# Kernel tuning notes

Measured on AMD Instinct MI355X. Metric: run time of the kernel, lower is better.

The kernel has to match this reference:

```python
import jax, jax.numpy as jnp
import numpy as np

# RVQECell configuration (matches init_kwargs)
I_SZ, W_SZ, STAGES, ORDER, DEGREE = 6, 12, 3, 2, 2
BIAS = float(np.pi / 2)
ANC = ORDER - 1                      # ancillas_for_order(order) = order - 1
N = I_SZ + W_SZ + ANC                # 19 qubits
B = 32
INOUT = list(range(I_SZ))            # lanes 0..5
WORK = list(range(I_SZ, I_SZ + W_SZ))  # lanes 6..17
C_CTRL = I_SZ + W_SZ - 1             # controls per neuron = 17


def setup_inputs() -> dict:
    key = jax.random.key(0)
    ks = jax.random.split(key, 9)
    s = 0.1  # small init keeps neuron angles in a well-conditioned range
    psi = jax.random.normal(ks[0], (B, 2 ** N), jnp.float32)
    psi = psi / jnp.linalg.norm(psi, axis=1, keepdims=True)  # normalized kets
    return {
        "batch": psi,
        "w_in1": jax.random.normal(ks[1], (W_SZ, C_CTRL), jnp.float32) * s,
        "w_in2": jax.random.normal(ks[2], (W_SZ, C_CTRL, C_CTRL), jnp.float32) * s,
        "w_u": jax.random.normal(ks[3], (STAGES, W_SZ), jnp.float32) * s,
        "w_k1": jax.random.normal(ks[4], (STAGES, W_SZ, C_CTRL), jnp.float32) * s,
        "w_k2": jax.random.normal(ks[5], (STAGES, W_SZ, C_CTRL, C_CTRL), jnp.float32) * s,
        "w_out1": jax.random.normal(ks[6], (I_SZ, C_CTRL), jnp.float32) * s,
        "w_out2": jax.random.normal(ks[7], (I_SZ, C_CTRL, C_CTRL), jnp.float32) * s,
        "inputs": jax.random.randint(ks[8], (B, I_SZ), 0, 2, dtype=jnp.int32),
    }


def _rot_y(state, lane, alpha):
    # real rotation [[cos a, -sin a], [sin a, cos a]] on qubit `lane`.
    ax = lane + 1  # +1 for batch axis; state shape [B] + [2]*N
    c, s = jnp.cos(alpha), jnp.sin(alpha)
    p0 = jax.lax.index_in_dim(state, 0, ax, keepdims=True)
    p1 = jax.lax.index_in_dim(state, 1, ax, keepdims=True)
    return jnp.concatenate([c * p0 - s * p1, s * p0 + c * p1], axis=ax)


def _neuron(state, outlane, th1, th2):
    # Fast (deterministic RUS) quantum neuron of given ORDER/DEGREE:
    # per control-basis-branch rotation of `outlane` by alpha(x),
    # phi(x) = bias + sum_i th1_i x_i + sum_{i<j} th2_ij x_i x_j (degree 2),
    # alpha = q^(order-1)(phi), q(t) = arctan(tan(t)^2), stable via arctan2.
    controls = [l for l in range(I_SZ + W_SZ) if l != outlane]
    Cn = len(controls)
    x = jnp.arange(2 ** Cn)
    shifts = jnp.arange(Cn - 1, -1, -1)
    bits = ((x[:, None] >> shifts[None, :]) & 1).astype(state.dtype)  # [2^Cn, Cn]
    phi = BIAS + bits @ th1
    if DEGREE >= 2:
        phi = phi + jnp.einsum('xi,ij,xj->x', bits, jnp.triu(th2, 1), bits)
    alpha = phi
    for _ in range(ORDER - 1):
        alpha = jnp.arctan2(jnp.sin(alpha) ** 2, jnp.cos(alpha) ** 2)
    shape = [1] + [2 if l in controls else 1 for l in range(N)]
    return _rot_y(state, outlane, alpha.reshape(shape))


def _bitflip(state_flat, inputs):
    # Vectorized batched BitFlipLayer: X on inout lane i where inputs[b,i]==1,
    # i.e. permute amplitudes by XOR of the flip mask (lane 0 most significant).
    shifts = (N - 1) - jnp.arange(I_SZ)
    f = jnp.sum(inputs.astype(jnp.int32) << shifts[None, :], axis=1)  # [B]
    idx = jnp.arange(2 ** N, dtype=jnp.int32)[None, :] ^ f[:, None]
    return jnp.take_along_axis(state_flat, idx, axis=1)


def reference(batch, w_in1, w_in2, w_u, w_k1, w_k2, w_out1, w_out2, inputs):
    psi = _bitflip(batch, inputs).reshape((B,) + (2,) * N)
    # input layer: one neuron per workspace lane
    for j, out in enumerate(WORK):
        psi = _neuron(psi, out, w_in1[j], w_in2[j])
    # kernel layer: stages x (UnitaryLayer(workspace) + neurons)
    for st in range(STAGES):
        for j, lane in enumerate(WORK):
            psi = _rot_y(psi, lane, w_u[st, j])
        for j, out in enumerate(WORK):
            psi = _neuron(psi, out, w_k1[st, j], w_k2[st, j])
    psi = _bitflip(psi.reshape(B, -1), inputs).reshape((B,) + (2,) * N)
    # output layer: one neuron per inout lane
    for j, out in enumerate(INOUT):
        psi = _neuron(psi, out, w_out1[j], w_out2[j])
    # measurement probabilities over inout lanes: marginal of |amp|^2
    probs = jnp.sum(psi ** 2, axis=tuple(range(1 + I_SZ, 1 + N))).reshape(B, -1)
    return probs, psi.reshape(B, -1)
```

## Files before the change

kernel.cpp:

```cpp
#include <hip/hip_runtime.h>
#include <math.h>


#define BIAS_F 1.57079632679489662f

typedef float v4f __attribute__((ext_vector_type(4)));

__device__ __forceinline__ float4 ntload4(const float* p) {
    v4f v = __builtin_nontemporal_load((const v4f*)p);
    return make_float4(v.x, v.y, v.z, v.w);
}
__device__ __forceinline__ void ntstore4(float* p, float4 f) {
    v4f v = {f.x, f.y, f.z, f.w};
    __builtin_nontemporal_store(v, (v4f*)p);
}

__device__ __forceinline__ int SW(int i) { return i ^ ((i >> 3) & 0x1C); }
__device__ __forceinline__ float4 ldsld4(const float* st, int i) {
    return *(const float4*)&st[SW(i)];
}
__device__ __forceinline__ void ldsst4(float* st, int i, float4 v) {
    *(float4*)&st[SW(i)] = v;
}

#define LD2(p) (*(const float2*)(p))
#define LD4(p) (*(const float4*)(p))

__device__ __forceinline__ void rot4(float4& A, float4& B, float4 e) {
    float ax = A.x, ay = A.y, az = A.z, aw = A.w;
    A.x = e.x * ax - e.y * B.x;  B.x = e.y * ax + e.x * B.x;
    A.y = e.x * ay - e.y * B.y;  B.y = e.y * ay + e.x * B.y;
    A.z = e.z * az - e.w * B.z;  B.z = e.w * az + e.z * B.z;
    A.w = e.z * aw - e.w * B.w;  B.w = e.w * aw + e.z * B.w;
}
__device__ __forceinline__ void rotq(float4& P, float c, float s) {
    float px = P.x, py = P.y;
    P.x = c * px - s * P.z;  P.z = s * px + c * P.z;
    P.y = c * py - s * P.w;  P.w = s * py + c * P.w;
}


__global__ __launch_bounds__(256) void tables_kernel(
    const float* __restrict__ w_in1, const float* __restrict__ w_in2,
    const float* __restrict__ w_k1,  const float* __restrict__ w_k2,
    const float* __restrict__ w_out1, const float* __restrict__ w_out2,
    float* __restrict__ tab)
{
    const int n = blockIdx.y;
    const int hi = blockIdx.x;
    const int tid = threadIdx.x;
    const float* th1;
    const float* th2;
    if (n < 12)      { th1 = w_in1 + n * 17;         th2 = w_in2 + n * 289; }
    else if (n < 48) { th1 = w_k1 + (n - 12) * 17;   th2 = w_k2 + (n - 12) * 289; }
    else             { th1 = w_out1 + (n - 48) * 17; th2 = w_out2 + (n - 48) * 289; }

    float phi_hi = BIAS_F;
    float C[8];
#pragma unroll
    for (int a = 0; a < 8; ++a) C[a] = th1[9 + a];
#pragma unroll
    for (int i = 0; i < 9; ++i) {
        if ((hi >> (8 - i)) & 1) {
            float acc = th1[i];
#pragma unroll
            for (int j = i + 1; j < 9; ++j)
                if ((hi >> (8 - j)) & 1) acc += th2[i * 17 + j];
            phi_hi += acc;
#pragma unroll
            for (int a = 0; a < 8; ++a) C[a] += th2[i * 17 + 9 + a];
        }
    }

    float bt[8];
#pragma unroll
    for (int j = 0; j < 8; ++j) bt[j] = (float)((tid >> (7 - j)) & 1);
    float phi = phi_hi;
#pragma unroll
    for (int a = 0; a < 8; ++a) {
        float acc = C[a];
#pragma unroll
        for (int b2 = a + 1; b2 < 8; ++b2) acc += bt[b2] * th2[(9 + a) * 17 + 9 + b2];
        phi += bt[a] * acc;
    }

    float sp, cp;
    sincosf(phi, &sp, &cp);
    float c2 = cp * cp, s2 = sp * sp;
    float d = c2 * c2 + s2 * s2;
    float r = rsqrtf(d);
    r = r * (1.5f - 0.5f * d * r * r);
    float2* dst = (float2*)tab + ((size_t)n * 131072 + (size_t)((hi << 8) | tid));
    *dst = make_float2(c2 * r, s2 * r);
}

template <int PA, bool NEUR>
__device__ __forceinline__ void pass_hi2(float* l0, float* l1, int t8,
    const float* tA, const float* tB, const float* tC,
    float cA, float sA, float cB, float sB, float cC, float sC)
{
    const int lowb = PA - 4;
    const int low = t8 & ((1 << lowb) - 1);
    const int high = t8 >> lowb;
    const int i0 = (high << (PA + 1)) | (low << 2);
    const int x0 = (high << (PA - 1)) | (low << 1);
    const int oa = 1 << PA, ob = oa >> 1, oc = oa >> 2;
    const int dhi = oa >> 2, dlo = oa >> 3;
    float4 ea00, ea01, ea10, ea11, eb00, eb01, eb10, eb11, ec00, ec01, ec10, ec11;
    if (NEUR) {
        ea00 = LD4(&tA[2 * x0]);            ea01 = LD4(&tA[2 * (x0 + dlo)]);
        ea10 = LD4(&tA[2 * (x0 + dhi)]);    ea11 = LD4(&tA[2 * (x0 + dhi + dlo)]);
        eb00 = LD4(&tB[2 * x0]);            eb01 = LD4(&tB[2 * (x0 + dlo)]);
        eb10 = LD4(&tB[2 * (x0 + dhi)]);    eb11 = LD4(&tB[2 * (x0 + dhi + dlo)]);
        ec00 = LD4(&tC[2 * x0]);            ec01 = LD4(&tC[2 * (x0 + dlo)]);
        ec10 = LD4(&tC[2 * (x0 + dhi)]);    ec11 = LD4(&tC[2 * (x0 + dhi + dlo)]);
    } else {
        ea00 = ea01 = ea10 = ea11 = make_float4(cA, sA, cA, sA);
        eb00 = eb01 = eb10 = eb11 = make_float4(cB, sB, cB, sB);
        ec00 = ec01 = ec10 = ec11 = make_float4(cC, sC, cC, sC);
    }
#pragma unroll
    for (int s = 0; s < 2; ++s) {
        float* sl = (s == 0) ? l0 : l1;
        float4 Q000 = ldsld4(sl, i0),            Q001 = ldsld4(sl, i0 + oc);
        float4 Q010 = ldsld4(sl, i0 + ob),       Q011 = ldsld4(sl, i0 + ob + oc);
        float4 Q100 = ldsld4(sl, i0 + oa),       Q101 = ldsld4(sl, i0 + oa + oc);
        float4 Q110 = ldsld4(sl, i0 + oa + ob),  Q111 = ldsld4(sl, i0 + oa + ob + oc);
        rot4(Q000, Q100, ea00); rot4(Q001, Q101, ea01);
        rot4(Q010, Q110, ea10); rot4(Q011, Q111, ea11);
        rot4(Q000, Q010, eb00); rot4(Q001, Q011, eb01);
        rot4(Q100, Q110, eb10); rot4(Q101, Q111, eb11);
        rot4(Q000, Q001, ec00); rot4(Q010, Q011, ec01);
        rot4(Q100, Q101, ec10); rot4(Q110, Q111, ec11);
        ldsst4(sl, i0, Q000);            ldsst4(sl, i0 + oc, Q001);
        ldsst4(sl, i0 + ob, Q010);       ldsst4(sl, i0 + ob + oc, Q011);
        ldsst4(sl, i0 + oa, Q100);       ldsst4(sl, i0 + oa + oc, Q101);
        ldsst4(sl, i0 + oa + ob, Q110);  ldsst4(sl, i0 + oa + ob + oc, Q111);
    }
}

template <bool NEUR>
__device__ __forceinline__ void pass_lo2(float* l0, float* l1, int t8,
    const float* tA, const float* tB, const float* tC,
    float cA, float sA, float cB, float sB, float cC, float sC)
{
    const int i0 = t8 << 5, x0 = t8 << 3;
    float4 ea0, ea1, ea2, ea3, eb0, eb1, eb2, eb3, ec0, ec1, ec2, ec3;
    if (NEUR) {
        ea0 = LD4(&tA[2 * x0]);      ea1 = LD4(&tA[2 * x0 + 4]);
        ea2 = LD4(&tA[2 * x0 + 8]);  ea3 = LD4(&tA[2 * x0 + 12]);
        eb0 = LD4(&tB[2 * x0]);      eb1 = LD4(&tB[2 * x0 + 4]);
        eb2 = LD4(&tB[2 * x0 + 8]);  eb3 = LD4(&tB[2 * x0 + 12]);
        ec0 = LD4(&tC[2 * x0]);      ec1 = LD4(&tC[2 * x0 + 4]);
        ec2 = LD4(&tC[2 * x0 + 8]);  ec3 = LD4(&tC[2 * x0 + 12]);
    } else {
        ea0 = ea1 = ea2 = ea3 = make_float4(cA, sA, cA, sA);
        eb0 = eb1 = eb2 = eb3 = make_float4(cB, sB, cB, sB);
        ec0 = ec1 = ec2 = ec3 = make_float4(cC, sC, cC, sC);
    }
#pragma unroll
    for (int s = 0; s < 2; ++s) {
        float* sl = (s == 0) ? l0 : l1;
        float4 Q0 = ldsld4(sl, i0),      Q1 = ldsld4(sl, i0 + 4);
        float4 Q2 = ldsld4(sl, i0 + 8),  Q3 = ldsld4(sl, i0 + 12);
        float4 Q4 = ldsld4(sl, i0 + 16), Q5 = ldsld4(sl, i0 + 20);
        float4 Q6 = ldsld4(sl, i0 + 24), Q7 = ldsld4(sl, i0 + 28);
        rot4(Q0, Q2, ea0); rot4(Q1, Q3, ea1); rot4(Q4, Q6, ea2); rot4(Q5, Q7, ea3);
        rot4(Q0, Q1, eb0); rot4(Q2, Q3, eb1); rot4(Q4, Q5, eb2); rot4(Q6, Q7, eb3);
        rotq(Q0, ec0.x, ec0.y); rotq(Q1, ec0.z, ec0.w);
        rotq(Q2, ec1.x, ec1.y); rotq(Q3, ec1.z, ec1.w);
        rotq(Q4, ec2.x, ec2.y); rotq(Q5, ec2.z, ec2.w);
        rotq(Q6, ec3.x, ec3.y); rotq(Q7, ec3.z, ec3.w);
        ldsst4(sl, i0, Q0);      ldsst4(sl, i0 + 4, Q1);
        ldsst4(sl, i0 + 8, Q2);  ldsst4(sl, i0 + 12, Q3);
        ldsst4(sl, i0 + 16, Q4); ldsst4(sl, i0 + 20, Q5);
        ldsst4(sl, i0 + 24, Q6); ldsst4(sl, i0 + 28, Q7);
    }
}

__global__ __launch_bounds__(256, 2) void main_kernel(
    const float* __restrict__ batch, const float* __restrict__ w_u,
    const int* __restrict__ inputs, const float* __restrict__ tab,
    float* __restrict__ psi, float* __restrict__ probs)
{
    __shared__ __align__(16) float lds[2][8192];
    const int t8 = threadIdx.x;
    const int blk = blockIdx.x;
    const int xcd = blk & 7;
    const int vt = (xcd << 3) | ((blk >> 3) & 7);
    const int pair = blk >> 6;

    if (blk == 0) {
        float4 z = make_float4(0.f, 0.f, 0.f, 0.f);
        *(float4*)&probs[t8 * 8] = z;
        *(float4*)&probs[t8 * 8 + 4] = z;
    }

    int bb[2], uu[2];
#pragma unroll
    for (int s = 0; s < 2; ++s) {
        int b = pair * 2 + s;
        int fb = 0;
#pragma unroll
        for (int i = 0; i < 6; ++i) fb |= (inputs[b * 6 + i] & 1) << (5 - i);
        bb[s] = b; uu[s] = vt ^ fb;
        const float* src = batch + ((size_t)b << 19) + ((size_t)uu[s] << 13);
#pragma unroll
        for (int k = 0; k < 8; ++k) {
            int i4 = (k * 256 + t8) * 4;
            float4 v = ntload4(&src[i4]);
            *(float4*)&lds[s][SW(i4)] = v;
        }
    }
    float* l0 = lds[0];
    float* l1 = lds[1];

    const float* tb = tab + ((size_t)vt << 12);
#define TN(j) (tb + (size_t)(j) * 262144)
#define BAR __syncthreads()
    BAR;
    pass_hi2<12, true>(l0, l1, t8, TN(0), TN(1), TN(2), 0,0,0,0,0,0);  BAR;
    pass_hi2<9,  true>(l0, l1, t8, TN(3), TN(4), TN(5), 0,0,0,0,0,0);  BAR;
    pass_hi2<6,  true>(l0, l1, t8, TN(6), TN(7), TN(8), 0,0,0,0,0,0);  BAR;
    pass_lo2<true>(l0, l1, t8, TN(9), TN(10), TN(11), 0,0,0,0,0,0);    BAR;

#pragma unroll 1
    for (int st2 = 0; st2 < 3; ++st2) {
        const float* wu = w_u + st2 * 12;
        float c0, s0, c1, s1, c2, s2;
        sincosf(wu[0], &s0, &c0); sincosf(wu[1], &s1, &c1); sincosf(wu[2], &s2, &c2);
        pass_hi2<12, false>(l0, l1, t8, 0,0,0, c0,s0, c1,s1, c2,s2);   BAR;
        sincosf(wu[3], &s0, &c0); sincosf(wu[4], &s1, &c1); sincosf(wu[5], &s2, &c2);
        pass_hi2<9, false>(l0, l1, t8, 0,0,0, c0,s0, c1,s1, c2,s2);    BAR;
        sincosf(wu[6], &s0, &c0); sincosf(wu[7], &s1, &c1); sincosf(wu[8], &s2, &c2);
        pass_hi2<6, false>(l0, l1, t8, 0,0,0, c0,s0, c1,s1, c2,s2);    BAR;
        sincosf(wu[9], &s0, &c0); sincosf(wu[10], &s1, &c1); sincosf(wu[11], &s2, &c2);
        pass_lo2<false>(l0, l1, t8, 0,0,0, c0,s0, c1,s1, c2,s2);       BAR;

        const int nb = 12 + st2 * 12;
        pass_hi2<12, true>(l0, l1, t8, TN(nb+0), TN(nb+1), TN(nb+2), 0,0,0,0,0,0); BAR;
        pass_hi2<9,  true>(l0, l1, t8, TN(nb+3), TN(nb+4), TN(nb+5), 0,0,0,0,0,0); BAR;
        pass_hi2<6,  true>(l0, l1, t8, TN(nb+6), TN(nb+7), TN(nb+8), 0,0,0,0,0,0); BAR;
        pass_lo2<true>(l0, l1, t8, TN(nb+9), TN(nb+10), TN(nb+11), 0,0,0,0,0,0);   BAR;
    }
#undef TN
#undef BAR

#pragma unroll
    for (int s = 0; s < 2; ++s) {
        float* dst = psi + ((size_t)bb[s] << 19) + ((size_t)uu[s] << 13);
#pragma unroll
        for (int k = 0; k < 8; ++k) {
            int i4 = (k * 256 + t8) * 4;
            float4 v = *(const float4*)&lds[s][SW(i4)];
            ntstore4(&dst[i4], v);
        }
    }
}

__global__ __launch_bounds__(256, 2) void out_kernel(
    const float* __restrict__ tab, float* __restrict__ psi,
    float* __restrict__ probs)
{
    __shared__ __align__(16) float ts[16384];
    const int tid = threadIdx.x;
    const int lane = tid & 63;
    const int wv = tid >> 6;
    const int b = blockIdx.x >> 5;
    const int c0 = (blockIdx.x & 31) << 8;
    float* gbase = psi + ((size_t)b << 19) + c0;

#pragma unroll
    for (int i = 0; i < 16; ++i) {
        int k = wv * 16 + i;
        float4 v = ntload4(&gbase[((size_t)k << 13) + lane * 4]);
        int f4 = lane ^ (k & 15);
        *(float4*)&ts[k * 256 + f4 * 4] = v;
    }
    __syncthreads();

    float a[64];
#pragma unroll
    for (int k = 0; k < 64; ++k) a[k] = ts[k * 256 + (tid ^ ((k & 15) << 2))];
    const int w12 = (c0 | tid) >> 1;

#define OSTAGE(J) { \
    const float* tj = tab + 2u * ((size_t)(48 + (J)) * 131072 + (size_t)w12); \
    _Pragma("unroll") \
    for (int h = 0; h < 2; ++h) { \
        float2 ev[16]; \
        _Pragma("unroll") \
        for (int m = 0; m < 16; ++m) ev[m] = LD2(&tj[(size_t)(h * 16 + m) << 13]); \
        _Pragma("unroll") \
        for (int m = 0; m < 16; ++m) { \
            const int mm = h * 16 + m; \
            const int q = 5 - (J); \
            const int k0 = ((mm >> q) << (q + 1)) | (mm & ((1 << q) - 1)); \
            const int k1 = k0 | (1 << q); \
            float2 e = ev[m]; \
            float A0 = a[k0], A1 = a[k1]; \
            a[k0] = e.x * A0 - e.y * A1; \
            a[k1] = e.y * A0 + e.x * A1; } } }
    OSTAGE(0) OSTAGE(1) OSTAGE(2) OSTAGE(3) OSTAGE(4) OSTAGE(5)
#undef OSTAGE

#pragma unroll
    for (int k = 0; k < 64; ++k) ts[k * 256 + (tid ^ ((k & 15) << 2))] = a[k];
    __syncthreads();

#pragma unroll
    for (int i = 0; i < 16; ++i) {
        int k = wv * 16 + i;
        int f4 = lane ^ (k & 15);
        float4 v = *(const float4*)&ts[k * 256 + f4 * 4];
        ntstore4(&gbase[((size_t)k << 13) + lane * 4], v);
    }

    const int k6 = tid & 63, seg = tid >> 6;
    float p = 0.f;
#pragma unroll
    for (int j = 0; j < 64; ++j) {
        int c = seg * 64 + ((j + k6) & 63);
        float v = ts[k6 * 256 + (c ^ ((k6 & 15) << 2))];
        p += v * v;
    }
    atomicAdd(&probs[b * 64 + k6], p);
}

extern "C" void kernel_launch(void* const* d_in, const int* in_sizes, int n_in,
                              void* d_out, int out_size, void* d_ws, size_t ws_size,
                              hipStream_t stream)
{
    const float* batch  = (const float*)d_in[0];
    const float* w_in1  = (const float*)d_in[1];
    const float* w_in2  = (const float*)d_in[2];
    const float* w_u    = (const float*)d_in[3];
    const float* w_k1   = (const float*)d_in[4];
    const float* w_k2   = (const float*)d_in[5];
    const float* w_out1 = (const float*)d_in[6];
    const float* w_out2 = (const float*)d_in[7];
    const int*   inputs = (const int*)d_in[8];
    float* probs = (float*)d_out;
    float* psi   = (float*)d_out + 2048;
    float* tab   = (float*)d_ws;

    tables_kernel<<<dim3(512, 54), 256, 0, stream>>>(w_in1, w_in2, w_k1, w_k2,
                                                     w_out1, w_out2, tab);
    main_kernel<<<1024, 256, 0, stream>>>(batch, w_u, inputs, tab, psi, probs);
    out_kernel<<<1024, 256, 0, stream>>>(tab, psi, probs);
}
```

Measured before the change: 328.3 us.

## Relayout output-neuron tables for coalesced LDS staging and batch table rows per block

The output-layer neuron tables are written in a transposed, rotated layout so that out_kernel can load two stages' tables with contiguous float4 copies into shared memory and read them from LDS. Before, each thread did strided global float2 loads. The tables kernel also now has each block loop over 8 high-index rows, which cuts its grid by 8x. This adds extra barriers in out_kernel and reuses the ts buffer, and the smaller table grid may lower occupancy.

```diff
diff --git a/kernel.cpp b/kernel.cpp
--- a/kernel.cpp
+++ b/kernel.cpp
@@ -47,7 +47,7 @@
     float* __restrict__ tab)
 {
     const int n = blockIdx.y;
-    const int hi = blockIdx.x;
+    const int bx = blockIdx.x;
     const int tid = threadIdx.x;
     const float* th1;
     const float* th2;
@@ -55,43 +55,57 @@
     else if (n < 48) { th1 = w_k1 + (n - 12) * 17;   th2 = w_k2 + (n - 12) * 289; }
     else             { th1 = w_out1 + (n - 48) * 17; th2 = w_out2 + (n - 48) * 289; }
 
-    float phi_hi = BIAS_F;
-    float C[8];
-#pragma unroll
-    for (int a = 0; a < 8; ++a) C[a] = th1[9 + a];
-#pragma unroll
-    for (int i = 0; i < 9; ++i) {
-        if ((hi >> (8 - i)) & 1) {
-            float acc = th1[i];
-#pragma unroll
-            for (int j = i + 1; j < 9; ++j)
-                if ((hi >> (8 - j)) & 1) acc += th2[i * 17 + j];
-            phi_hi += acc;
-#pragma unroll
-            for (int a = 0; a < 8; ++a) C[a] += th2[i * 17 + 9 + a];
-        }
-    }
-
     float bt[8];
 #pragma unroll
     for (int j = 0; j < 8; ++j) bt[j] = (float)((tid >> (7 - j)) & 1);
-    float phi = phi_hi;
-#pragma unroll
-    for (int a = 0; a < 8; ++a) {
-        float acc = C[a];
-#pragma unroll
-        for (int b2 = a + 1; b2 < 8; ++b2) acc += bt[b2] * th2[(9 + a) * 17 + 9 + b2];
-        phi += bt[a] * acc;
-    }
-
-    float sp, cp;
-    sincosf(phi, &sp, &cp);
-    float c2 = cp * cp, s2 = sp * sp;
-    float d = c2 * c2 + s2 * s2;
-    float r = rsqrtf(d);
-    r = r * (1.5f - 0.5f * d * r * r);
-    float2* dst = (float2*)tab + ((size_t)n * 131072 + (size_t)((hi << 8) | tid));
-    *dst = make_float2(c2 * r, s2 * r);
+
+#pragma unroll 1
+    for (int k = 0; k < 8; ++k) {
+        const int hi = bx * 8 + k;
+
+        float phi_hi = BIAS_F;
+        float C[8];
+#pragma unroll
+        for (int a = 0; a < 8; ++a) C[a] = th1[9 + a];
+#pragma unroll
+        for (int i = 0; i < 9; ++i) {
+            if ((hi >> (8 - i)) & 1) {
+                float acc = th1[i];
+#pragma unroll
+                for (int j = i + 1; j < 9; ++j)
+                    if ((hi >> (8 - j)) & 1) acc += th2[i * 17 + j];
+                phi_hi += acc;
+#pragma unroll
+                for (int a = 0; a < 8; ++a) C[a] += th2[i * 17 + 9 + a];
+            }
+        }
+
+        float phi = phi_hi;
+#pragma unroll
+        for (int a = 0; a < 8; ++a) {
+            float acc = C[a];
+#pragma unroll
+            for (int b2 = a + 1; b2 < 8; ++b2) acc += bt[b2] * th2[(9 + a) * 17 + 9 + b2];
+            phi += bt[a] * acc;
+        }
+
+        float sp, cp;
+        sincosf(phi, &sp, &cp);
+        float c2 = cp * cp, s2 = sp * sp;
+        float d = c2 * c2 + s2 * s2;
+        float r = rsqrtf(d);
+        r = r * (1.5f - 0.5f * d * r * r);
+
+        size_t idx;
+        if (n < 48) {
+            idx = (size_t)n * 131072 + (size_t)((hi << 8) | tid);
+        } else {
+            const int m = hi >> 4;
+            const int w12 = ((hi & 15) << 8) | tid;
+            idx = (size_t)n * 131072 + (size_t)(w12 * 32 + ((m + w12) & 31));
+        }
+        ((float2*)tab)[idx] = make_float2(c2 * r, s2 * r);
+    }
 }
 
 template <int PA, bool NEUR>
@@ -282,28 +296,44 @@
     float a[64];
 #pragma unroll
     for (int k = 0; k < 64; ++k) a[k] = ts[k * 256 + (tid ^ ((k & 15) << 2))];
-    const int w12 = (c0 | tid) >> 1;
-
-#define OSTAGE(J) { \
-    const float* tj = tab + 2u * ((size_t)(48 + (J)) * 131072 + (size_t)w12); \
+
+    const int w12l = tid >> 1;
+    const size_t tbase = (size_t)(c0 >> 1) * 32;
+    const float2* tab2 = (const float2*)tab;
+    float2* ts2 = (float2*)ts;
+
+#define OSTAGE(J, TSEL) { \
+    const int q = 5 - (J); \
     _Pragma("unroll") \
-    for (int h = 0; h < 2; ++h) { \
-        float2 ev[16]; \
-        _Pragma("unroll") \
-        for (int m = 0; m < 16; ++m) ev[m] = LD2(&tj[(size_t)(h * 16 + m) << 13]); \
-        _Pragma("unroll") \
-        for (int m = 0; m < 16; ++m) { \
-            const int mm = h * 16 + m; \
-            const int q = 5 - (J); \
-            const int k0 = ((mm >> q) << (q + 1)) | (mm & ((1 << q) - 1)); \
-            const int k1 = k0 | (1 << q); \
-            float2 e = ev[m]; \
-            float A0 = a[k0], A1 = a[k1]; \
-            a[k0] = e.x * A0 - e.y * A1; \
-            a[k1] = e.y * A0 + e.x * A1; } } }
-    OSTAGE(0) OSTAGE(1) OSTAGE(2) OSTAGE(3) OSTAGE(4) OSTAGE(5)
+    for (int m = 0; m < 32; ++m) { \
+        float2 e = ts2[(TSEL) * 4096 + w12l * 32 + ((m + w12l) & 31)]; \
+        const int k0 = ((m >> q) << (q + 1)) | (m & ((1 << q) - 1)); \
+        const int k1 = k0 | (1 << q); \
+        float A0 = a[k0], A1 = a[k1]; \
+        a[k0] = e.x * A0 - e.y * A1; \
+        a[k1] = e.y * A0 + e.x * A1; } }
+
+#pragma unroll 1
+    for (int p = 0; p < 3; ++p) {
+        __syncthreads();
+        const float4* g0 = (const float4*)(tab2 + (size_t)(48 + 2 * p) * 131072 + tbase);
+        const float4* g1 = (const float4*)(tab2 + (size_t)(49 + 2 * p) * 131072 + tbase);
+        float4* d4 = (float4*)ts;
+#pragma unroll 4
+        for (int it = 0; it < 8; ++it) {
+            d4[it * 256 + tid]        = g0[it * 256 + tid];
+            d4[2048 + it * 256 + tid] = g1[it * 256 + tid];
+        }
+        __syncthreads();
+        switch (p) {
+            case 0: OSTAGE(0, 0) OSTAGE(1, 1) break;
+            case 1: OSTAGE(2, 0) OSTAGE(3, 1) break;
+            default: OSTAGE(4, 0) OSTAGE(5, 1) break;
+        }
+    }
 #undef OSTAGE
 
+    __syncthreads();
 #pragma unroll
     for (int k = 0; k < 64; ++k) ts[k * 256 + (tid ^ ((k & 15) << 2))] = a[k];
     __syncthreads();
@@ -344,8 +374,8 @@
     float* psi   = (float*)d_out + 2048;
     float* tab   = (float*)d_ws;
 
-    tables_kernel<<<dim3(512, 54), 256, 0, stream>>>(w_in1, w_in2, w_k1, w_k2,
-                                                     w_out1, w_out2, tab);
+    tables_kernel<<<dim3(64, 54), 256, 0, stream>>>(w_in1, w_in2, w_k1, w_k2,
+                                                    w_out1, w_out2, tab);
     main_kernel<<<1024, 256, 0, stream>>>(batch, w_u, inputs, tab, psi, probs);
     out_kernel<<<1024, 256, 0, stream>>>(tab, psi, probs);
 }
```

Result: slower. 374.4 us (+14.1%).

## Fuse three kernels into persistent mega-kernel with software grid barriers

Applied to the files above, without the earlier changes.

Merges the table-building, main state-evolution and output-neuron kernels into a single persistent kernel of 512 blocks. Each block does two work units per phase, and atomic-counter grid barriers (reset by a memset) separate the phases. The aim is to remove kernel launch gaps and tail effects between the three launches. In exchange, occupancy is halved relative to 1024-block launches, and correctness depends on all 512 blocks being co-resident; if they are not, the barriers deadlock. Table computation now loops over 54 neurons serially per block.

```diff
diff --git a/kernel.cpp b/kernel.cpp
--- a/kernel.cpp
+++ b/kernel.cpp
@@ -39,60 +39,17 @@
     P.y = c * py - s * P.w;  P.w = s * py + c * P.w;
 }
 
-
-__global__ __launch_bounds__(256) void tables_kernel(
-    const float* __restrict__ w_in1, const float* __restrict__ w_in2,
-    const float* __restrict__ w_k1,  const float* __restrict__ w_k2,
-    const float* __restrict__ w_out1, const float* __restrict__ w_out2,
-    float* __restrict__ tab)
-{
-    const int n = blockIdx.y;
-    const int hi = blockIdx.x;
-    const int tid = threadIdx.x;
-    const float* th1;
-    const float* th2;
-    if (n < 12)      { th1 = w_in1 + n * 17;         th2 = w_in2 + n * 289; }
-    else if (n < 48) { th1 = w_k1 + (n - 12) * 17;   th2 = w_k2 + (n - 12) * 289; }
-    else             { th1 = w_out1 + (n - 48) * 17; th2 = w_out2 + (n - 48) * 289; }
-
-    float phi_hi = BIAS_F;
-    float C[8];
-#pragma unroll
-    for (int a = 0; a < 8; ++a) C[a] = th1[9 + a];
-#pragma unroll
-    for (int i = 0; i < 9; ++i) {
-        if ((hi >> (8 - i)) & 1) {
-            float acc = th1[i];
-#pragma unroll
-            for (int j = i + 1; j < 9; ++j)
-                if ((hi >> (8 - j)) & 1) acc += th2[i * 17 + j];
-            phi_hi += acc;
-#pragma unroll
-            for (int a = 0; a < 8; ++a) C[a] += th2[i * 17 + 9 + a];
-        }
-    }
-
-    float bt[8];
-#pragma unroll
-    for (int j = 0; j < 8; ++j) bt[j] = (float)((tid >> (7 - j)) & 1);
-    float phi = phi_hi;
-#pragma unroll
-    for (int a = 0; a < 8; ++a) {
-        float acc = C[a];
-#pragma unroll
-        for (int b2 = a + 1; b2 < 8; ++b2) acc += bt[b2] * th2[(9 + a) * 17 + 9 + b2];
-        phi += bt[a] * acc;
-    }
-
-    float sp, cp;
-    sincosf(phi, &sp, &cp);
-    float c2 = cp * cp, s2 = sp * sp;
-    float d = c2 * c2 + s2 * s2;
-    float r = rsqrtf(d);
-    r = r * (1.5f - 0.5f * d * r * r);
-    float2* dst = (float2*)tab + ((size_t)n * 131072 + (size_t)((hi << 8) | tid));
-    *dst = make_float2(c2 * r, s2 * r);
-}
+__device__ __forceinline__ void grid_barrier(unsigned* bar, unsigned nb) {
+    __syncthreads();
+    if (threadIdx.x == 0) {
+        __hip_atomic_fetch_add(bar, 1u, __ATOMIC_ACQ_REL, __HIP_MEMORY_SCOPE_AGENT);
+        while (__hip_atomic_load(bar, __ATOMIC_ACQUIRE, __HIP_MEMORY_SCOPE_AGENT) < nb) {
+            __builtin_amdgcn_s_sleep(16);
+        }
+    }
+    __syncthreads();
+}
+
 
 template <int PA, bool NEUR>
 __device__ __forceinline__ void pass_hi2(float* l0, float* l1, int t8,
@@ -178,111 +135,175 @@
     }
 }
 
-__global__ __launch_bounds__(256, 2) void main_kernel(
-    const float* __restrict__ batch, const float* __restrict__ w_u,
-    const int* __restrict__ inputs, const float* __restrict__ tab,
+__global__ __launch_bounds__(256, 2) void mega_kernel(
+    const float* __restrict__ batch,
+    const float* __restrict__ w_in1, const float* __restrict__ w_in2,
+    const float* __restrict__ w_u,
+    const float* __restrict__ w_k1,  const float* __restrict__ w_k2,
+    const float* __restrict__ w_out1, const float* __restrict__ w_out2,
+    const int* __restrict__ inputs,
+    float* __restrict__ tab, unsigned* __restrict__ bar,
     float* __restrict__ psi, float* __restrict__ probs)
 {
-    __shared__ __align__(16) float lds[2][8192];
-    const int t8 = threadIdx.x;
+    __shared__ __align__(16) float lds[16384];
+    const int tid = threadIdx.x;
     const int blk = blockIdx.x;
-    const int xcd = blk & 7;
-    const int vt = (xcd << 3) | ((blk >> 3) & 7);
-    const int pair = blk >> 6;
-
+
+    {
+        const int hi = blk;
+        float bt[8];
+#pragma unroll
+        for (int j = 0; j < 8; ++j) bt[j] = (float)((tid >> (7 - j)) & 1);
+
+#pragma unroll 1
+        for (int n = 0; n < 54; ++n) {
+            const float* th1;
+            const float* th2;
+            if (n < 12)      { th1 = w_in1 + n * 17;         th2 = w_in2 + n * 289; }
+            else if (n < 48) { th1 = w_k1 + (n - 12) * 17;   th2 = w_k2 + (n - 12) * 289; }
+            else             { th1 = w_out1 + (n - 48) * 17; th2 = w_out2 + (n - 48) * 289; }
+
+            float phi_hi = BIAS_F;
+            float C[8];
+#pragma unroll
+            for (int a = 0; a < 8; ++a) C[a] = th1[9 + a];
+#pragma unroll
+            for (int i = 0; i < 9; ++i) {
+                if ((hi >> (8 - i)) & 1) {
+                    float acc = th1[i];
+#pragma unroll
+                    for (int j = i + 1; j < 9; ++j)
+                        if ((hi >> (8 - j)) & 1) acc += th2[i * 17 + j];
+                    phi_hi += acc;
+#pragma unroll
+                    for (int a = 0; a < 8; ++a) C[a] += th2[i * 17 + 9 + a];
+                }
+            }
+            float phi = phi_hi;
+#pragma unroll
+            for (int a = 0; a < 8; ++a) {
+                float acc = C[a];
+#pragma unroll
+                for (int b2 = a + 1; b2 < 8; ++b2)
+                    acc += bt[b2] * th2[(9 + a) * 17 + 9 + b2];
+                phi += bt[a] * acc;
+            }
+            float sp, cp;
+            sincosf(phi, &sp, &cp);
+            float c2 = cp * cp, s2 = sp * sp;
+            float d = c2 * c2 + s2 * s2;
+            float r = rsqrtf(d);
+            r = r * (1.5f - 0.5f * d * r * r);
+            float2* dst = (float2*)tab +
+                ((size_t)n * 131072 + (size_t)((hi << 8) | tid));
+            *dst = make_float2(c2 * r, s2 * r);
+        }
+    }
     if (blk == 0) {
         float4 z = make_float4(0.f, 0.f, 0.f, 0.f);
-        *(float4*)&probs[t8 * 8] = z;
-        *(float4*)&probs[t8 * 8 + 4] = z;
-    }
-
-    int bb[2], uu[2];
-#pragma unroll
-    for (int s = 0; s < 2; ++s) {
-        int b = pair * 2 + s;
-        int fb = 0;
-#pragma unroll
-        for (int i = 0; i < 6; ++i) fb |= (inputs[b * 6 + i] & 1) << (5 - i);
-        bb[s] = b; uu[s] = vt ^ fb;
-        const float* src = batch + ((size_t)b << 19) + ((size_t)uu[s] << 13);
-#pragma unroll
-        for (int k = 0; k < 8; ++k) {
-            int i4 = (k * 256 + t8) * 4;
-            float4 v = ntload4(&src[i4]);
-            *(float4*)&lds[s][SW(i4)] = v;
-        }
-    }
-    float* l0 = lds[0];
-    float* l1 = lds[1];
-
-    const float* tb = tab + ((size_t)vt << 12);
+        *(float4*)&probs[tid * 8] = z;
+        *(float4*)&probs[tid * 8 + 4] = z;
+    }
+    grid_barrier(bar + 0, 512u);
+
+    float* l0 = lds;
+    float* l1 = lds + 8192;
+#pragma unroll 1
+    for (int u2 = 0; u2 < 2; ++u2) {
+        const int unit = blk + u2 * 512;
+        const int xcd = unit & 7;
+        const int vt = (xcd << 3) | ((unit >> 3) & 7);
+        const int pair = unit >> 6;
+        const int t8 = tid;
+
+        int bb[2], uu[2];
+#pragma unroll
+        for (int s = 0; s < 2; ++s) {
+            int b = pair * 2 + s;
+            int fb = 0;
+#pragma unroll
+            for (int i = 0; i < 6; ++i) fb |= (inputs[b * 6 + i] & 1) << (5 - i);
+            bb[s] = b; uu[s] = vt ^ fb;
+            const float* src = batch + ((size_t)b << 19) + ((size_t)uu[s] << 13);
+            float* sl = (s == 0) ? l0 : l1;
+#pragma unroll
+            for (int k = 0; k < 8; ++k) {
+                int i4 = (k * 256 + t8) * 4;
+                float4 v = ntload4(&src[i4]);
+                *(float4*)&sl[SW(i4)] = v;
+            }
+        }
+
+        const float* tb = tab + ((size_t)vt << 12);
 #define TN(j) (tb + (size_t)(j) * 262144)
 #define BAR __syncthreads()
-    BAR;
-    pass_hi2<12, true>(l0, l1, t8, TN(0), TN(1), TN(2), 0,0,0,0,0,0);  BAR;
-    pass_hi2<9,  true>(l0, l1, t8, TN(3), TN(4), TN(5), 0,0,0,0,0,0);  BAR;
-    pass_hi2<6,  true>(l0, l1, t8, TN(6), TN(7), TN(8), 0,0,0,0,0,0);  BAR;
-    pass_lo2<true>(l0, l1, t8, TN(9), TN(10), TN(11), 0,0,0,0,0,0);    BAR;
+        BAR;
+        pass_hi2<12, true>(l0, l1, t8, TN(0), TN(1), TN(2), 0,0,0,0,0,0);  BAR;
+        pass_hi2<9,  true>(l0, l1, t8, TN(3), TN(4), TN(5), 0,0,0,0,0,0);  BAR;
+        pass_hi2<6,  true>(l0, l1, t8, TN(6), TN(7), TN(8), 0,0,0,0,0,0);  BAR;
+        pass_lo2<true>(l0, l1, t8, TN(9), TN(10), TN(11), 0,0,0,0,0,0);    BAR;
 
 #pragma unroll 1
-    for (int st2 = 0; st2 < 3; ++st2) {
-        const float* wu = w_u + st2 * 12;
-        float c0, s0, c1, s1, c2, s2;
-        sincosf(wu[0], &s0, &c0); sincosf(wu[1], &s1, &c1); sincosf(wu[2], &s2, &c2);
-        pass_hi2<12, false>(l0, l1, t8, 0,0,0, c0,s0, c1,s1, c2,s2);   BAR;
-        sincosf(wu[3], &s0, &c0); sincosf(wu[4], &s1, &c1); sincosf(wu[5], &s2, &c2);
-        pass_hi2<9, false>(l0, l1, t8, 0,0,0, c0,s0, c1,s1, c2,s2);    BAR;
-        sincosf(wu[6], &s0, &c0); sincosf(wu[7], &s1, &c1); sincosf(wu[8], &s2, &c2);
-        pass_hi2<6, false>(l0, l1, t8, 0,0,0, c0,s0, c1,s1, c2,s2);    BAR;
-        sincosf(wu[9], &s0, &c0); sincosf(wu[10], &s1, &c1); sincosf(wu[11], &s2, &c2);
-        pass_lo2<false>(l0, l1, t8, 0,0,0, c0,s0, c1,s1, c2,s2);       BAR;
-
-        const int nb = 12 + st2 * 12;
-        pass_hi2<12, true>(l0, l1, t8, TN(nb+0), TN(nb+1), TN(nb+2), 0,0,0,0,0,0); BAR;
-        pass_hi2<9,  true>(l0, l1, t8, TN(nb+3), TN(nb+4), TN(nb+5), 0,0,0,0,0,0); BAR;
-        pass_hi2<6,  true>(l0, l1, t8, TN(nb+6), TN(nb+7), TN(nb+8), 0,0,0,0,0,0); BAR;
-        pass_lo2<true>(l0, l1, t8, TN(nb+9), TN(nb+10), TN(nb+11), 0,0,0,0,0,0);   BAR;
-    }
+        for (int st2 = 0; st2 < 3; ++st2) {
+            const float* wu = w_u + st2 * 12;
+            float c0, s0, c1, s1, c2, s2;
+            sincosf(wu[0], &s0, &c0); sincosf(wu[1], &s1, &c1); sincosf(wu[2], &s2, &c2);
+            pass_hi2<12, false>(l0, l1, t8, 0,0,0, c0,s0, c1,s1, c2,s2);   BAR;
+            sincosf(wu[3], &s0, &c0); sincosf(wu[4], &s1, &c1); sincosf(wu[5], &s2, &c2);
+            pass_hi2<9, false>(l0, l1, t8, 0,0,0, c0,s0, c1,s1, c2,s2);    BAR;
+            sincosf(wu[6], &s0, &c0); sincosf(wu[7], &s1, &c1); sincosf(wu[8], &s2, &c2);
+            pass_hi2<6, false>(l0, l1, t8, 0,0,0, c0,s0, c1,s1, c2,s2);    BAR;
+            sincosf(wu[9], &s0, &c0); sincosf(wu[10], &s1, &c1); sincosf(wu[11], &s2, &c2);
+            pass_lo2<false>(l0, l1, t8, 0,0,0, c0,s0, c1,s1, c2,s2);       BAR;
+
+            const int nb = 12 + st2 * 12;
+            pass_hi2<12, true>(l0, l1, t8, TN(nb+0), TN(nb+1), TN(nb+2), 0,0,0,0,0,0); BAR;
+            pass_hi2<9,  true>(l0, l1, t8, TN(nb+3), TN(nb+4), TN(nb+5), 0,0,0,0,0,0); BAR;
+            pass_hi2<6,  true>(l0, l1, t8, TN(nb+6), TN(nb+7), TN(nb+8), 0,0,0,0,0,0); BAR;
+            pass_lo2<true>(l0, l1, t8, TN(nb+9), TN(nb+10), TN(nb+11), 0,0,0,0,0,0);   BAR;
+        }
 #undef TN
 #undef BAR
 
 #pragma unroll
-    for (int s = 0; s < 2; ++s) {
-        float* dst = psi + ((size_t)bb[s] << 19) + ((size_t)uu[s] << 13);
-#pragma unroll
-        for (int k = 0; k < 8; ++k) {
-            int i4 = (k * 256 + t8) * 4;
-            float4 v = *(const float4*)&lds[s][SW(i4)];
-            ntstore4(&dst[i4], v);
-        }
-    }
-}
-
-__global__ __launch_bounds__(256, 2) void out_kernel(
-    const float* __restrict__ tab, float* __restrict__ psi,
-    float* __restrict__ probs)
-{
-    __shared__ __align__(16) float ts[16384];
-    const int tid = threadIdx.x;
-    const int lane = tid & 63;
-    const int wv = tid >> 6;
-    const int b = blockIdx.x >> 5;
-    const int c0 = (blockIdx.x & 31) << 8;
-    float* gbase = psi + ((size_t)b << 19) + c0;
-
-#pragma unroll
-    for (int i = 0; i < 16; ++i) {
-        int k = wv * 16 + i;
-        float4 v = ntload4(&gbase[((size_t)k << 13) + lane * 4]);
-        int f4 = lane ^ (k & 15);
-        *(float4*)&ts[k * 256 + f4 * 4] = v;
-    }
-    __syncthreads();
-
-    float a[64];
-#pragma unroll
-    for (int k = 0; k < 64; ++k) a[k] = ts[k * 256 + (tid ^ ((k & 15) << 2))];
-    const int w12 = (c0 | tid) >> 1;
+        for (int s = 0; s < 2; ++s) {
+            float* dst = psi + ((size_t)bb[s] << 19) + ((size_t)uu[s] << 13);
+            float* sl = (s == 0) ? l0 : l1;
+#pragma unroll
+            for (int k = 0; k < 8; ++k) {
+                int i4 = (k * 256 + t8) * 4;
+                float4 v = *(const float4*)&sl[SW(i4)];
+                ntstore4(&dst[i4], v);
+            }
+        }
+        __syncthreads();
+    }
+    grid_barrier(bar + 1, 512u);
+
+    float* ts = lds;
+#pragma unroll 1
+    for (int u2 = 0; u2 < 2; ++u2) {
+        __syncthreads();
+        const int unit = blk + u2 * 512;
+        const int lane = tid & 63;
+        const int wv = tid >> 6;
+        const int b = unit >> 5;
+        const int c0 = (unit & 31) << 8;
+        float* gbase = psi + ((size_t)b << 19) + c0;
+
+#pragma unroll
+        for (int i = 0; i < 16; ++i) {
+            int k = wv * 16 + i;
+            float4 v = ntload4(&gbase[((size_t)k << 13) + lane * 4]);
+            int f4 = lane ^ (k & 15);
+            *(float4*)&ts[k * 256 + f4 * 4] = v;
+        }
+        __syncthreads();
+
+        float a[64];
+#pragma unroll
+        for (int k = 0; k < 64; ++k) a[k] = ts[k * 256 + (tid ^ ((k & 15) << 2))];
+        const int w12 = (c0 | tid) >> 1;
 
 #define OSTAGE(J) { \
     const float* tj = tab + 2u * ((size_t)(48 + (J)) * 131072 + (size_t)w12); \
@@ -301,30 +322,31 @@
             float A0 = a[k0], A1 = a[k1]; \
             a[k0] = e.x * A0 - e.y * A1; \
             a[k1] = e.y * A0 + e.x * A1; } } }
-    OSTAGE(0) OSTAGE(1) OSTAGE(2) OSTAGE(3) OSTAGE(4) OSTAGE(5)
+        OSTAGE(0) OSTAGE(1) OSTAGE(2) OSTAGE(3) OSTAGE(4) OSTAGE(5)
 #undef OSTAGE
 
 #pragma unroll
-    for (int k = 0; k < 64; ++k) ts[k * 256 + (tid ^ ((k & 15) << 2))] = a[k];
-    __syncthreads();
-
-#pragma unroll
-    for (int i = 0; i < 16; ++i) {
-        int k = wv * 16 + i;
-        int f4 = lane ^ (k & 15);
-        float4 v = *(const float4*)&ts[k * 256 + f4 * 4];
-        ntstore4(&gbase[((size_t)k << 13) + lane * 4], v);
-    }
-
-    const int k6 = tid & 63, seg = tid >> 6;
-    float p = 0.f;
-#pragma unroll
-    for (int j = 0; j < 64; ++j) {
-        int c = seg * 64 + ((j + k6) & 63);
-        float v = ts[k6 * 256 + (c ^ ((k6 & 15) << 2))];
-        p += v * v;
-    }
-    atomicAdd(&probs[b * 64 + k6], p);
+        for (int k = 0; k < 64; ++k) ts[k * 256 + (tid ^ ((k & 15) << 2))] = a[k];
+        __syncthreads();
+
+#pragma unroll
+        for (int i = 0; i < 16; ++i) {
+            int k = wv * 16 + i;
+            int f4 = lane ^ (k & 15);
+            float4 v = *(const float4*)&ts[k * 256 + f4 * 4];
+            ntstore4(&gbase[((size_t)k << 13) + lane * 4], v);
+        }
+
+        const int k6 = tid & 63, seg = tid >> 6;
+        float p = 0.f;
+#pragma unroll
+        for (int j = 0; j < 64; ++j) {
+            int c = seg * 64 + ((j + k6) & 63);
+            float v = ts[k6 * 256 + (c ^ ((k6 & 15) << 2))];
+            p += v * v;
+        }
+        atomicAdd(&probs[b * 64 + k6], p);
+    }
 }
 
 extern "C" void kernel_launch(void* const* d_in, const int* in_sizes, int n_in,
@@ -343,9 +365,10 @@
     float* probs = (float*)d_out;
     float* psi   = (float*)d_out + 2048;
     float* tab   = (float*)d_ws;
-
-    tables_kernel<<<dim3(512, 54), 256, 0, stream>>>(w_in1, w_in2, w_k1, w_k2,
-                                                     w_out1, w_out2, tab);
-    main_kernel<<<1024, 256, 0, stream>>>(batch, w_u, inputs, tab, psi, probs);
-    out_kernel<<<1024, 256, 0, stream>>>(tab, psi, probs);
-}
+    unsigned* bar = (unsigned*)((char*)d_ws + (size_t)54 * 1024 * 1024);
+
+    hipMemsetAsync(bar, 0, 2 * sizeof(unsigned), stream);
+    mega_kernel<<<512, 256, 0, stream>>>(batch, w_in1, w_in2, w_u, w_k1, w_k2,
+                                         w_out1, w_out2, inputs, tab, bar,
+                                         psi, probs);
+}
```

Measured after the change: 786.0 us. 139% more time.

## Prefetch neuron tables into registers one pass ahead and fuse unitary pass

Applied to the files above, without the earlier changes.

Table loading is split from the LDS compute passes, so the next pass's neuron angle table is loaded into registers while the current pass runs. This double-buffers across the barrier and hides global-load latency. Each stage's single-qubit unitary rotations are reordered, which is valid because rotations on different qubits commute. That lets the lane-12 unitary rotations fuse into the following lane-12 neuron pass, removing one LDS round trip and one barrier per stage. Launch bounds drop to one block per CU minimum to allow the extra live registers, which risks lower occupancy.

```diff
diff --git a/kernel.cpp b/kernel.cpp
--- a/kernel.cpp
+++ b/kernel.cpp
@@ -94,31 +94,51 @@
     *dst = make_float2(c2 * r, s2 * r);
 }
 
-template <int PA, bool NEUR>
-__device__ __forceinline__ void pass_hi2(float* l0, float* l1, int t8,
-    const float* tA, const float* tB, const float* tC,
+struct TabRegs { float4 r[12]; };
+
+template <int PA>
+__device__ __forceinline__ TabRegs tload_hi(const float* tA, const float* tB,
+                                            const float* tC, int t8)
+{
+    const int lowb = PA - 4;
+    const int low = t8 & ((1 << lowb) - 1);
+    const int high = t8 >> lowb;
+    const int x0 = (high << (PA - 1)) | (low << 1);
+    const int dhi = (1 << PA) >> 2, dlo = (1 << PA) >> 3;
+    TabRegs t;
+    t.r[0]  = LD4(&tA[2 * x0]);            t.r[1]  = LD4(&tA[2 * (x0 + dlo)]);
+    t.r[2]  = LD4(&tA[2 * (x0 + dhi)]);    t.r[3]  = LD4(&tA[2 * (x0 + dhi + dlo)]);
+    t.r[4]  = LD4(&tB[2 * x0]);            t.r[5]  = LD4(&tB[2 * (x0 + dlo)]);
+    t.r[6]  = LD4(&tB[2 * (x0 + dhi)]);    t.r[7]  = LD4(&tB[2 * (x0 + dhi + dlo)]);
+    t.r[8]  = LD4(&tC[2 * x0]);            t.r[9]  = LD4(&tC[2 * (x0 + dlo)]);
+    t.r[10] = LD4(&tC[2 * (x0 + dhi)]);    t.r[11] = LD4(&tC[2 * (x0 + dhi + dlo)]);
+    return t;
+}
+
+__device__ __forceinline__ TabRegs tload_lo(const float* tA, const float* tB,
+                                            const float* tC, int t8)
+{
+    const int x0 = t8 << 3;
+    TabRegs t;
+    t.r[0]  = LD4(&tA[2 * x0]);      t.r[1]  = LD4(&tA[2 * x0 + 4]);
+    t.r[2]  = LD4(&tA[2 * x0 + 8]);  t.r[3]  = LD4(&tA[2 * x0 + 12]);
+    t.r[4]  = LD4(&tB[2 * x0]);      t.r[5]  = LD4(&tB[2 * x0 + 4]);
+    t.r[6]  = LD4(&tB[2 * x0 + 8]);  t.r[7]  = LD4(&tB[2 * x0 + 12]);
+    t.r[8]  = LD4(&tC[2 * x0]);      t.r[9]  = LD4(&tC[2 * x0 + 4]);
+    t.r[10] = LD4(&tC[2 * x0 + 8]);  t.r[11] = LD4(&tC[2 * x0 + 12]);
+    return t;
+}
+
+template <int PA, bool NEUR, bool UNI>
+__device__ __forceinline__ void compute_hi(float* l0, float* l1, int t8,
+    const TabRegs& tr,
     float cA, float sA, float cB, float sB, float cC, float sC)
 {
     const int lowb = PA - 4;
     const int low = t8 & ((1 << lowb) - 1);
     const int high = t8 >> lowb;
     const int i0 = (high << (PA + 1)) | (low << 2);
-    const int x0 = (high << (PA - 1)) | (low << 1);
     const int oa = 1 << PA, ob = oa >> 1, oc = oa >> 2;
-    const int dhi = oa >> 2, dlo = oa >> 3;
-    float4 ea00, ea01, ea10, ea11, eb00, eb01, eb10, eb11, ec00, ec01, ec10, ec11;
-    if (NEUR) {
-        ea00 = LD4(&tA[2 * x0]);            ea01 = LD4(&tA[2 * (x0 + dlo)]);
-        ea10 = LD4(&tA[2 * (x0 + dhi)]);    ea11 = LD4(&tA[2 * (x0 + dhi + dlo)]);
-        eb00 = LD4(&tB[2 * x0]);            eb01 = LD4(&tB[2 * (x0 + dlo)]);
-        eb10 = LD4(&tB[2 * (x0 + dhi)]);    eb11 = LD4(&tB[2 * (x0 + dhi + dlo)]);
-        ec00 = LD4(&tC[2 * x0]);            ec01 = LD4(&tC[2 * (x0 + dlo)]);
-        ec10 = LD4(&tC[2 * (x0 + dhi)]);    ec11 = LD4(&tC[2 * (x0 + dhi + dlo)]);
-    } else {
-        ea00 = ea01 = ea10 = ea11 = make_float4(cA, sA, cA, sA);
-        eb00 = eb01 = eb10 = eb11 = make_float4(cB, sB, cB, sB);
-        ec00 = ec01 = ec10 = ec11 = make_float4(cC, sC, cC, sC);
-    }
 #pragma unroll
     for (int s = 0; s < 2; ++s) {
         float* sl = (s == 0) ? l0 : l1;
@@ -126,12 +146,25 @@
         float4 Q010 = ldsld4(sl, i0 + ob),       Q011 = ldsld4(sl, i0 + ob + oc);
         float4 Q100 = ldsld4(sl, i0 + oa),       Q101 = ldsld4(sl, i0 + oa + oc);
         float4 Q110 = ldsld4(sl, i0 + oa + ob),  Q111 = ldsld4(sl, i0 + oa + ob + oc);
-        rot4(Q000, Q100, ea00); rot4(Q001, Q101, ea01);
-        rot4(Q010, Q110, ea10); rot4(Q011, Q111, ea11);
-        rot4(Q000, Q010, eb00); rot4(Q001, Q011, eb01);
-        rot4(Q100, Q110, eb10); rot4(Q101, Q111, eb11);
-        rot4(Q000, Q001, ec00); rot4(Q010, Q011, ec01);
-        rot4(Q100, Q101, ec10); rot4(Q110, Q111, ec11);
+        if (UNI || !NEUR) {
+            float4 eA = make_float4(cA, sA, cA, sA);
+            rot4(Q000, Q100, eA); rot4(Q001, Q101, eA);
+            rot4(Q010, Q110, eA); rot4(Q011, Q111, eA);
+            float4 eB = make_float4(cB, sB, cB, sB);
+            rot4(Q000, Q010, eB); rot4(Q001, Q011, eB);
+            rot4(Q100, Q110, eB); rot4(Q101, Q111, eB);
+            float4 eC = make_float4(cC, sC, cC, sC);
+            rot4(Q000, Q001, eC); rot4(Q010, Q011, eC);
+            rot4(Q100, Q101, eC); rot4(Q110, Q111, eC);
+        }
+        if (NEUR) {
+            rot4(Q000, Q100, tr.r[0]); rot4(Q001, Q101, tr.r[1]);
+            rot4(Q010, Q110, tr.r[2]); rot4(Q011, Q111, tr.r[3]);
+            rot4(Q000, Q010, tr.r[4]); rot4(Q001, Q011, tr.r[5]);
+            rot4(Q100, Q110, tr.r[6]); rot4(Q101, Q111, tr.r[7]);
+            rot4(Q000, Q001, tr.r[8]);  rot4(Q010, Q011, tr.r[9]);
+            rot4(Q100, Q101, tr.r[10]); rot4(Q110, Q111, tr.r[11]);
+        }
         ldsst4(sl, i0, Q000);            ldsst4(sl, i0 + oc, Q001);
         ldsst4(sl, i0 + ob, Q010);       ldsst4(sl, i0 + ob + oc, Q011);
         ldsst4(sl, i0 + oa, Q100);       ldsst4(sl, i0 + oa + oc, Q101);
@@ -140,24 +173,11 @@
 }
 
 template <bool NEUR>
-__device__ __forceinline__ void pass_lo2(float* l0, float* l1, int t8,
-    const float* tA, const float* tB, const float* tC,
+__device__ __forceinline__ void compute_lo(float* l0, float* l1, int t8,
+    const TabRegs& tr,
     float cA, float sA, float cB, float sB, float cC, float sC)
 {
-    const int i0 = t8 << 5, x0 = t8 << 3;
-    float4 ea0, ea1, ea2, ea3, eb0, eb1, eb2, eb3, ec0, ec1, ec2, ec3;
-    if (NEUR) {
-        ea0 = LD4(&tA[2 * x0]);      ea1 = LD4(&tA[2 * x0 + 4]);
-        ea2 = LD4(&tA[2 * x0 + 8]);  ea3 = LD4(&tA[2 * x0 + 12]);
-        eb0 = LD4(&tB[2 * x0]);      eb1 = LD4(&tB[2 * x0 + 4]);
-        eb2 = LD4(&tB[2 * x0 + 8]);  eb3 = LD4(&tB[2 * x0 + 12]);
-        ec0 = LD4(&tC[2 * x0]);      ec1 = LD4(&tC[2 * x0 + 4]);
-        ec2 = LD4(&tC[2 * x0 + 8]);  ec3 = LD4(&tC[2 * x0 + 12]);
-    } else {
-        ea0 = ea1 = ea2 = ea3 = make_float4(cA, sA, cA, sA);
-        eb0 = eb1 = eb2 = eb3 = make_float4(cB, sB, cB, sB);
-        ec0 = ec1 = ec2 = ec3 = make_float4(cC, sC, cC, sC);
-    }
+    const int i0 = t8 << 5;
 #pragma unroll
     for (int s = 0; s < 2; ++s) {
         float* sl = (s == 0) ? l0 : l1;
@@ -165,12 +185,23 @@
         float4 Q2 = ldsld4(sl, i0 + 8),  Q3 = ldsld4(sl, i0 + 12);
         float4 Q4 = ldsld4(sl, i0 + 16), Q5 = ldsld4(sl, i0 + 20);
         float4 Q6 = ldsld4(sl, i0 + 24), Q7 = ldsld4(sl, i0 + 28);
-        rot4(Q0, Q2, ea0); rot4(Q1, Q3, ea1); rot4(Q4, Q6, ea2); rot4(Q5, Q7, ea3);
-        rot4(Q0, Q1, eb0); rot4(Q2, Q3, eb1); rot4(Q4, Q5, eb2); rot4(Q6, Q7, eb3);
-        rotq(Q0, ec0.x, ec0.y); rotq(Q1, ec0.z, ec0.w);
-        rotq(Q2, ec1.x, ec1.y); rotq(Q3, ec1.z, ec1.w);
-        rotq(Q4, ec2.x, ec2.y); rotq(Q5, ec2.z, ec2.w);
-        rotq(Q6, ec3.x, ec3.y); rotq(Q7, ec3.z, ec3.w);
+        if (NEUR) {
+            rot4(Q0, Q2, tr.r[0]); rot4(Q1, Q3, tr.r[1]);
+            rot4(Q4, Q6, tr.r[2]); rot4(Q5, Q7, tr.r[3]);
+            rot4(Q0, Q1, tr.r[4]); rot4(Q2, Q3, tr.r[5]);
+            rot4(Q4, Q5, tr.r[6]); rot4(Q6, Q7, tr.r[7]);
+            rotq(Q0, tr.r[8].x,  tr.r[8].y);  rotq(Q1, tr.r[8].z,  tr.r[8].w);
+            rotq(Q2, tr.r[9].x,  tr.r[9].y);  rotq(Q3, tr.r[9].z,  tr.r[9].w);
+            rotq(Q4, tr.r[10].x, tr.r[10].y); rotq(Q5, tr.r[10].z, tr.r[10].w);
+            rotq(Q6, tr.r[11].x, tr.r[11].y); rotq(Q7, tr.r[11].z, tr.r[11].w);
+        } else {
+            float4 eA = make_float4(cA, sA, cA, sA);
+            rot4(Q0, Q2, eA); rot4(Q1, Q3, eA); rot4(Q4, Q6, eA); rot4(Q5, Q7, eA);
+            float4 eB = make_float4(cB, sB, cB, sB);
+            rot4(Q0, Q1, eB); rot4(Q2, Q3, eB); rot4(Q4, Q5, eB); rot4(Q6, Q7, eB);
+            rotq(Q0, cC, sC); rotq(Q1, cC, sC); rotq(Q2, cC, sC); rotq(Q3, cC, sC);
+            rotq(Q4, cC, sC); rotq(Q5, cC, sC); rotq(Q6, cC, sC); rotq(Q7, cC, sC);
+        }
         ldsst4(sl, i0, Q0);      ldsst4(sl, i0 + 4, Q1);
         ldsst4(sl, i0 + 8, Q2);  ldsst4(sl, i0 + 12, Q3);
         ldsst4(sl, i0 + 16, Q4); ldsst4(sl, i0 + 20, Q5);
@@ -178,7 +209,7 @@
     }
 }
 
-__global__ __launch_bounds__(256, 2) void main_kernel(
+__global__ __launch_bounds__(256, 1) void main_kernel(
     const float* __restrict__ batch, const float* __restrict__ w_u,
     const int* __restrict__ inputs, const float* __restrict__ tab,
     float* __restrict__ psi, float* __restrict__ probs)
@@ -218,30 +249,41 @@
     const float* tb = tab + ((size_t)vt << 12);
 #define TN(j) (tb + (size_t)(j) * 262144)
 #define BAR __syncthreads()
+
+    TabRegs A, B;
+    A = tload_hi<12>(TN(0), TN(1), TN(2), t8);
     BAR;
-    pass_hi2<12, true>(l0, l1, t8, TN(0), TN(1), TN(2), 0,0,0,0,0,0);  BAR;
-    pass_hi2<9,  true>(l0, l1, t8, TN(3), TN(4), TN(5), 0,0,0,0,0,0);  BAR;
-    pass_hi2<6,  true>(l0, l1, t8, TN(6), TN(7), TN(8), 0,0,0,0,0,0);  BAR;
-    pass_lo2<true>(l0, l1, t8, TN(9), TN(10), TN(11), 0,0,0,0,0,0);    BAR;
+    B = tload_hi<9>(TN(3), TN(4), TN(5), t8);
+    compute_hi<12, true, false>(l0, l1, t8, A, 0,0,0,0,0,0);  BAR;
+    A = tload_hi<6>(TN(6), TN(7), TN(8), t8);
+    compute_hi<9, true, false>(l0, l1, t8, B, 0,0,0,0,0,0);   BAR;
+    B = tload_lo(TN(9), TN(10), TN(11), t8);
+    compute_hi<6, true, false>(l0, l1, t8, A, 0,0,0,0,0,0);   BAR;
+    A = tload_hi<12>(TN(12), TN(13), TN(14), t8);
+    compute_lo<true>(l0, l1, t8, B, 0,0,0,0,0,0);             BAR;
 
 #pragma unroll 1
     for (int st2 = 0; st2 < 3; ++st2) {
         const float* wu = w_u + st2 * 12;
+        const int nb = 12 + st2 * 12;
         float c0, s0, c1, s1, c2, s2;
+        sincosf(wu[3], &s0, &c0); sincosf(wu[4], &s1, &c1); sincosf(wu[5], &s2, &c2);
+        compute_hi<9, false, false>(l0, l1, t8, A, c0,s0, c1,s1, c2,s2);  BAR;
+        sincosf(wu[6], &s0, &c0); sincosf(wu[7], &s1, &c1); sincosf(wu[8], &s2, &c2);
+        compute_hi<6, false, false>(l0, l1, t8, A, c0,s0, c1,s1, c2,s2);  BAR;
+        sincosf(wu[9], &s0, &c0); sincosf(wu[10], &s1, &c1); sincosf(wu[11], &s2, &c2);
+        compute_lo<false>(l0, l1, t8, A, c0,s0, c1,s1, c2,s2);            BAR;
+
         sincosf(wu[0], &s0, &c0); sincosf(wu[1], &s1, &c1); sincosf(wu[2], &s2, &c2);
-        pass_hi2<12, false>(l0, l1, t8, 0,0,0, c0,s0, c1,s1, c2,s2);   BAR;
-        sincosf(wu[3], &s0, &c0); sincosf(wu[4], &s1, &c1); sincosf(wu[5], &s2, &c2);
-        pass_hi2<9, false>(l0, l1, t8, 0,0,0, c0,s0, c1,s1, c2,s2);    BAR;
-        sincosf(wu[6], &s0, &c0); sincosf(wu[7], &s1, &c1); sincosf(wu[8], &s2, &c2);
-        pass_hi2<6, false>(l0, l1, t8, 0,0,0, c0,s0, c1,s1, c2,s2);    BAR;
-        sincosf(wu[9], &s0, &c0); sincosf(wu[10], &s1, &c1); sincosf(wu[11], &s2, &c2);
-        pass_lo2<false>(l0, l1, t8, 0,0,0, c0,s0, c1,s1, c2,s2);       BAR;
-
-        const int nb = 12 + st2 * 12;
-        pass_hi2<12, true>(l0, l1, t8, TN(nb+0), TN(nb+1), TN(nb+2), 0,0,0,0,0,0); BAR;
-        pass_hi2<9,  true>(l0, l1, t8, TN(nb+3), TN(nb+4), TN(nb+5), 0,0,0,0,0,0); BAR;
-        pass_hi2<6,  true>(l0, l1, t8, TN(nb+6), TN(nb+7), TN(nb+8), 0,0,0,0,0,0); BAR;
-        pass_lo2<true>(l0, l1, t8, TN(nb+9), TN(nb+10), TN(nb+11), 0,0,0,0,0,0);   BAR;
+        B = tload_hi<9>(TN(nb+3), TN(nb+4), TN(nb+5), t8);
+        compute_hi<12, true, true>(l0, l1, t8, A, c0,s0, c1,s1, c2,s2);   BAR;
+        A = tload_hi<6>(TN(nb+6), TN(nb+7), TN(nb+8), t8);
+        compute_hi<9, true, false>(l0, l1, t8, B, 0,0,0,0,0,0);           BAR;
+        B = tload_lo(TN(nb+9), TN(nb+10), TN(nb+11), t8);
+        compute_hi<6, true, false>(l0, l1, t8, A, 0,0,0,0,0,0);           BAR;
+        if (st2 < 2)
+            A = tload_hi<12>(TN(nb+12), TN(nb+13), TN(nb+14), t8);
+        compute_lo<true>(l0, l1, t8, B, 0,0,0,0,0,0);                     BAR;
     }
 #undef TN
 #undef BAR
```

After: 368.0 us. 12.1% more time.
